# Kernel tuning notes

Measured on AMD Instinct MI355X. Metric: run time of the kernel, lower is better.

## Reference

```python
import jax, jax.numpy as jnp
import numpy as np

EMB = 768          # MineModel.emb_size
HEADS = 4          # Mi hard-codes n_heads=4 for QTLayer
DK = EMB // HEADS  # 192
H_NEED = 3         # MineModel need_num_heads
QLEN = 10000
TLEN = 3000
EG = 100000        # give edges (before head replication)
EI = 100000        # inter_1 / inter_2 edges
NLAYERS = 2


def setup_inputs() -> dict:
    key = jax.random.key(0)
    ks = jax.random.split(key, 20)
    f = lambda k, s: jax.random.normal(k, s, dtype=jnp.float32) * 0.02
    return {
        'q_emb': jax.random.normal(ks[0], (QLEN, EMB), jnp.float32),
        't_emb': jax.random.normal(ks[1], (TLEN, EMB), jnp.float32),
        'give_src': jax.random.randint(ks[2], (EG,), 0, TLEN),
        'give_dst': jax.random.randint(ks[3], (EG,), 0, QLEN),
        'i1_src': jax.random.randint(ks[4], (EI,), 0, TLEN),
        'i1_dst': jax.random.randint(ks[5], (EI,), 0, TLEN),
        'i2_src': jax.random.randint(ks[6], (EI,), 0, TLEN),
        'i2_dst': jax.random.randint(ks[7], (EI,), 0, TLEN),
        'Wq_enc': f(ks[8], (EMB, EMB * H_NEED)),
        'bq_enc': jnp.zeros((EMB * H_NEED,), jnp.float32),
        'Wc': f(ks[9], (EMB, 10)),
        'bc': jnp.zeros((10,), jnp.float32),
        'centers': f(ks[10], (10, EMB)),
        'kW': f(ks[11], (NLAYERS, 2, EMB, EMB)),
        'kb': jnp.zeros((NLAYERS, 2, EMB), jnp.float32),
        'qW': f(ks[12], (NLAYERS, 2, EMB, EMB)),
        'qb': jnp.zeros((NLAYERS, 2, EMB), jnp.float32),
        'vW': f(ks[13], (NLAYERS, 2, EMB, EMB)),
        'vb': jnp.zeros((NLAYERS, 2, EMB), jnp.float32),
        'rel_att': f(ks[14], (NLAYERS, 3, HEADS, DK, DK)),
        'rel_msg': f(ks[15], (NLAYERS, 3, HEADS, DK, DK)),
        'rel_pri': jnp.ones((NLAYERS, 3, HEADS), jnp.float32),
        'Wout': f(ks[16], (EMB, EMB)),
        'bout': jnp.zeros((EMB,), jnp.float32),
    }


def _edge_softmax(score, dst, n_dst):
    # softmax over incoming edges of each destination node, per head
    m = jax.ops.segment_max(score, dst, num_segments=n_dst)      # [N, H]
    e = jnp.exp(score - m[dst])
    s = jax.ops.segment_sum(e, dst, num_segments=n_dst)
    return e / s[dst]


def _rel(k_src, v_src, q_dst, src, dst, n_dst, ratt, rmsg, rpri):
    # HGT relation: relation-specific K/V transform, edge dot-attention, scatter-sum
    k = jnp.einsum('nhd,hde->nhe', k_src, ratt)                  # [Nsrc, H, DK]
    v = jnp.einsum('nhd,hde->nhe', v_src, rmsg)
    score = jnp.einsum('ehd,ehd->eh', q_dst[dst], k[src]) * rpri / jnp.sqrt(jnp.float32(DK))
    a = _edge_softmax(score, dst, n_dst)                         # [E, H]
    return jax.ops.segment_sum(v[src] * a[:, :, None], dst, num_segments=n_dst)


def reference(q_emb, t_emb, give_src, give_dst, i1_src, i1_dst, i2_src, i2_dst,
              Wq_enc, bq_enc, Wc, bc, centers, kW, kb, qW, qb, vW, vb,
              rel_att, rel_msg, rel_pri, Wout, bout):
    n_q = QLEN * H_NEED
    # replicate 'give' edges per model-level head (cached graph construction)
    g_src = jnp.tile(give_src, H_NEED)
    g_dst = jnp.concatenate([give_dst + QLEN * i for i in range(H_NEED)])

    # question encoder -> split heads along feature dim, concat along rows
    q_hs = q_emb @ Wq_enc + bq_enc                               # [Q, EMB*H]
    q_h = q_hs.reshape(QLEN, H_NEED, EMB).transpose(1, 0, 2).reshape(n_q, EMB)
    q_h = q_h + jnp.tile(q_emb, (H_NEED, 1))
    assign = jax.nn.softmax(q_h @ Wc + bc, axis=-1)              # [n_q, 10]
    q_h = q_h + assign @ centers

    h_tag, h_q = t_emb, q_h
    for l in range(NLAYERS):
        k_tag = (h_tag @ kW[l, 0] + kb[l, 0]).reshape(-1, HEADS, DK)
        v_tag = (h_tag @ vW[l, 0] + vb[l, 0]).reshape(-1, HEADS, DK)
        q_tag = (h_tag @ qW[l, 0] + qb[l, 0]).reshape(-1, HEADS, DK)
        q_que = (h_q @ qW[l, 1] + qb[l, 1]).reshape(-1, HEADS, DK)
        t_q = _rel(k_tag, v_tag, q_que, g_src, g_dst, n_q,
                   rel_att[l, 0], rel_msg[l, 0], rel_pri[l, 0])
        t1 = _rel(k_tag, v_tag, q_tag, i1_src, i1_dst, TLEN,
                  rel_att[l, 1], rel_msg[l, 1], rel_pri[l, 1])
        t2 = _rel(k_tag, v_tag, q_tag, i2_src, i2_dst, TLEN,
                  rel_att[l, 2], rel_msg[l, 2], rel_pri[l, 2])
        # cross_reducer='mean' over the two tag->tag relations; residual add
        h_tag = (0.5 * (t1 + t2)).reshape(-1, EMB) + h_tag
        h_q = t_q.reshape(-1, EMB) + h_q

    ques_heads = h_q @ Wout + bout                               # [H*Q, EMB]
    tags = h_tag @ Wout + bout                                   # [T, EMB]
    # torch.split(.., q_len, dim=0) + stack(dim=1) -> [Q, H, EMB]
    ques = ques_heads.reshape(H_NEED, QLEN, EMB).transpose(1, 0, 2)
    return ques, tags
```

## Files before the change

### kernel.cpp

```cpp
#include <hip/hip_runtime.h>

#define QLEN 10000
#define TLEN 3000
#define EMB 768
#define HNEED 3
#define NQ (QLEN * HNEED)
#define EG 100000
#define EI 100000
#define DKH 192
#define NHEADS 4

namespace {

typedef unsigned short u16;
typedef unsigned char u8;
typedef unsigned int u32;
typedef __attribute__((ext_vector_type(8))) short bf16x8;
typedef __attribute__((ext_vector_type(4))) float f32x4;
typedef __attribute__((ext_vector_type(2))) float f32x2;

constexpr float SCALE = 0.07216878364870322f;
constexpr long long WS = (long long)EMB * EMB;
constexpr long long RS = (long long)DKH * DKH;

__device__ inline u16 f2bf(float f) {
  unsigned u = __float_as_uint(f);
  unsigned r = (u + 0x7FFFu + ((u >> 16) & 1u)) >> 16;
  return (u16)r;
}
__device__ inline float bf2f(u16 h) {
  return __uint_as_float((unsigned)h << 16);
}
__device__ inline u8 f2fp8(float f) {
  u32 pk = __builtin_amdgcn_cvt_pk_fp8_f32(f, f, 0, false);
  return (u8)(pk & 0xFF);
}
__device__ inline void decode12(const u32* p, float* o) {
#pragma unroll
  for (int t = 0; t < 3; ++t) {
    u32 w = p[t];
    f32x2 lo = __builtin_amdgcn_cvt_pk_f32_fp8(w, false);
    f32x2 hi = __builtin_amdgcn_cvt_pk_f32_fp8(w, true);
    o[t * 4 + 0] = lo[0]; o[t * 4 + 1] = lo[1];
    o[t * 4 + 2] = hi[0]; o[t * 4 + 3] = hi[1];
  }
}
__device__ inline f32x2 bfx2(u32 w) {
  f32x2 r;
  r[0] = __uint_as_float(w << 16);
  r[1] = __uint_as_float(w & 0xFFFF0000u);
  return r;
}

__device__ inline void gload_lds16(const u16* g, u16* s) {
  __builtin_amdgcn_global_load_lds(
      (const __attribute__((address_space(1))) unsigned*)g,
      (__attribute__((address_space(3))) unsigned*)s, 16, 0, 0);
}

template <int EPI, int OUT, int MODE>
__global__ __launch_bounds__(256) void gemm_bf16(
    const u16* __restrict__ A, int lda, long long sAz,
    const u16* __restrict__ Bt, int ldb, long long sBz,
    void* __restrict__ Cv, int ldc, long long sCz,
    const float* __restrict__ bias, const u16* __restrict__ extra,
    int M, int N, int K)
{
  __shared__ __align__(16) u16 As[3][4096];
  __shared__ __align__(16) u16 Bs[3][4096];
  const int z = blockIdx.z;
  float* Cf = (float*)Cv;
  u16* Ch = (u16*)Cv;
  u8* C8 = (u8*)Cv;
  if (MODE == 1) {
    const int lr = z >> 3, kv = (z >> 2) & 1, h = z & 3;
    const int l = lr >= 3;
    A += (long long)z * RS;
    Bt = (kv ? extra : Bt) + (long long)(l * 2) * WS + h * 192;
    Ch = (u16*)Cv + (long long)lr * 1536 * 768 + (long long)(kv * 768 + h * 192) * 768;
  } else {
    A += (long long)z * sAz;
    Bt += (long long)z * sBz;
    Cf += (long long)z * sCz;
    Ch += (long long)z * sCz;
    C8 += (long long)z * sCz;
  }
  const int gx = gridDim.x;
  const int nwg = gx * gridDim.y;
  const int orig = blockIdx.y * gx + blockIdx.x;
  const int qq = nwg >> 3, rr = nwg & 7;
  const int xc = orig & 7, ix = orig >> 3;
  const int swz = (xc < rr ? xc * (qq + 1) : rr * (qq + 1) + (xc - rr) * qq) + ix;
  const int by = swz / gx, bx = swz - by * gx;
  const int bm = by * 128, bn = bx * 128;

  const int tid = threadIdx.x;
  const int w = tid >> 6, l = tid & 63;
  const int wr = w >> 1, wc = w & 1;
  const int l16 = l & 15, lk = l >> 4;
  const int srow = tid >> 2;
  const int scol = (((tid & 3) ^ ((srow >> 1) & 3))) * 8;
  const int rchunk = (lk ^ ((l16 >> 1) & 3));

  int r0 = bm + srow;      if (r0 > M - 1) r0 = M - 1;
  int r1 = bm + srow + 64; if (r1 > M - 1) r1 = M - 1;
  int c0 = bn + srow;      if (c0 > N - 1) c0 = N - 1;
  int c1 = bn + srow + 64; if (c1 > N - 1) c1 = N - 1;
  const u16* pa0 = A + (long long)r0 * lda + scol;
  const u16* pa1 = A + (long long)r1 * lda + scol;
  const u16* pb0 = Bt + (long long)c0 * ldb + scol;
  const u16* pb1 = Bt + (long long)c1 * ldb + scol;

  int aoff[4], boff[4];
#pragma unroll
  for (int m = 0; m < 4; ++m) {
    aoff[m] = (wr * 64 + m * 16 + l16) * 32 + rchunk * 8;
    boff[m] = (wc * 64 + m * 16 + l16) * 32 + rchunk * 8;
  }

  f32x4 acc[4][4] = {};
  const int nt = K / 32;

  auto stage = [&](int buf, int k0) {
    gload_lds16(pa0 + k0, &As[buf][w * 512]);
    gload_lds16(pa1 + k0, &As[buf][w * 512 + 2048]);
    gload_lds16(pb0 + k0, &Bs[buf][w * 512]);
    gload_lds16(pb1 + k0, &Bs[buf][w * 512 + 2048]);
  };

  stage(0, 0);
  stage(1, 32);
  int cur = 0, sb = 2;
  for (int t = 0; t < nt; ++t) {
    if (t < nt - 1)
      asm volatile("s_waitcnt vmcnt(4)" ::: "memory");
    else
      asm volatile("s_waitcnt vmcnt(0)" ::: "memory");
    __builtin_amdgcn_s_barrier();
    __builtin_amdgcn_sched_barrier(0);
    if (t + 2 < nt) {
      stage(sb, (t + 2) * 32);
      if (++sb == 3) sb = 0;
    }
    bf16x8 af[4], bf[4];
#pragma unroll
    for (int m = 0; m < 4; ++m)
      af[m] = *(const bf16x8*)&As[cur][aoff[m]];
#pragma unroll
    for (int n = 0; n < 4; ++n)
      bf[n] = *(const bf16x8*)&Bs[cur][boff[n]];
    __builtin_amdgcn_s_setprio(1);
#pragma unroll
    for (int m = 0; m < 4; ++m)
#pragma unroll
      for (int n = 0; n < 4; ++n)
        acc[m][n] = __builtin_amdgcn_mfma_f32_16x16x32_bf16(af[m], bf[n], acc[m][n], 0, 0, 0);
    __builtin_amdgcn_s_setprio(0);
    if (++cur == 3) cur = 0;
  }

#pragma unroll
  for (int m = 0; m < 4; ++m) {
#pragma unroll
    for (int j = 0; j < 4; ++j) {
      int grow = bm + wr * 64 + m * 16 + lk * 4 + j;
      if (grow >= M) continue;
#pragma unroll
      for (int n = 0; n < 4; ++n) {
        int gcol = bn + wc * 64 + n * 16 + l16;
        if (gcol >= N) continue;
        float val = acc[m][n][j] + (bias ? bias[gcol] : 0.f);
        if (EPI == 0) {
          if (OUT == 0)
            Cf[(long long)grow * ldc + gcol] = val;
          else if (OUT == 1)
            Ch[(long long)grow * ldc + gcol] = f2bf(val);
          else
            C8[(long long)grow * ldc + gcol] = f2fp8(val);
        } else if (EPI == 1) {
          int h = gcol / EMB, c = gcol - h * EMB;
          Ch[((long long)h * QLEN + grow) * EMB + c] =
              f2bf(val + bf2f(extra[(long long)grow * EMB + c]));
        } else {
          if (grow < NQ) {
            int i2 = grow % QLEN, h = grow / QLEN;
            Cf[((long long)i2 * HNEED + h) * EMB + gcol] = val;
          } else {
            Cf[(long long)grow * EMB + gcol] = val;
          }
        }
      }
    }
  }
}

struct PackJobs {
  const u16* A[5];
  const u16* Bt[5];
  void* C[5];
  const float* bias[5];
  int M[5];
  int nx[5];
  int ldc[5];
  int out[5];
  int start[6];
};

__global__ __launch_bounds__(256) void gemm_pack(PackJobs Jb)
{
  const int nwg = Jb.start[5];
  const int orig = blockIdx.x;
  const int qq = nwg >> 3, rr = nwg & 7;
  const int xc = orig & 7, ix = orig >> 3;
  const int swz = (xc < rr ? xc * (qq + 1) : rr * (qq + 1) + (xc - rr) * qq) + ix;
  int j = 0;
  while (swz >= Jb.start[j + 1]) ++j;
  const int local = swz - Jb.start[j];
  const int nx = Jb.nx[j];
  const int by = local / nx, bx = local - by * nx;
  const int bm = by * 128, bn = bx * 128;
  const int M = Jb.M[j];
  const int ldc = Jb.ldc[j];
  const int outk = Jb.out[j];
  const u16* A = Jb.A[j];
  const u16* Bt = Jb.Bt[j];
  const float* bias = Jb.bias[j];
  u16* Ch = (u16*)Jb.C[j];
  u8* C8 = (u8*)Jb.C[j];

  __shared__ __align__(16) u16 As[3][4096];
  __shared__ __align__(16) u16 Bs[3][4096];

  const int tid = threadIdx.x;
  const int w = tid >> 6, l = tid & 63;
  const int wr = w >> 1, wc = w & 1;
  const int l16 = l & 15, lk = l >> 4;
  const int srow = tid >> 2;
  const int scol = (((tid & 3) ^ ((srow >> 1) & 3))) * 8;
  const int rchunk = (lk ^ ((l16 >> 1) & 3));

  int r0 = bm + srow;      if (r0 > M - 1) r0 = M - 1;
  int r1 = bm + srow + 64; if (r1 > M - 1) r1 = M - 1;
  const int c0 = bn + srow;
  const int c1 = bn + srow + 64;
  const u16* pa0 = A + (long long)r0 * 768 + scol;
  const u16* pa1 = A + (long long)r1 * 768 + scol;
  const u16* pb0 = Bt + (long long)c0 * 768 + scol;
  const u16* pb1 = Bt + (long long)c1 * 768 + scol;

  int aoff[4], boff[4];
#pragma unroll
  for (int m = 0; m < 4; ++m) {
    aoff[m] = (wr * 64 + m * 16 + l16) * 32 + rchunk * 8;
    boff[m] = (wc * 64 + m * 16 + l16) * 32 + rchunk * 8;
  }

  f32x4 acc[4][4] = {};
  const int nt = 24;

  auto stage = [&](int buf, int k0) {
    gload_lds16(pa0 + k0, &As[buf][w * 512]);
    gload_lds16(pa1 + k0, &As[buf][w * 512 + 2048]);
    gload_lds16(pb0 + k0, &Bs[buf][w * 512]);
    gload_lds16(pb1 + k0, &Bs[buf][w * 512 + 2048]);
  };

  stage(0, 0);
  stage(1, 32);
  int cur = 0, sb = 2;
  for (int t = 0; t < nt; ++t) {
    if (t < nt - 1)
      asm volatile("s_waitcnt vmcnt(4)" ::: "memory");
    else
      asm volatile("s_waitcnt vmcnt(0)" ::: "memory");
    __builtin_amdgcn_s_barrier();
    __builtin_amdgcn_sched_barrier(0);
    if (t + 2 < nt) {
      stage(sb, (t + 2) * 32);
      if (++sb == 3) sb = 0;
    }
    bf16x8 af[4], bf[4];
#pragma unroll
    for (int m = 0; m < 4; ++m)
      af[m] = *(const bf16x8*)&As[cur][aoff[m]];
#pragma unroll
    for (int n = 0; n < 4; ++n)
      bf[n] = *(const bf16x8*)&Bs[cur][boff[n]];
    __builtin_amdgcn_s_setprio(1);
#pragma unroll
    for (int m = 0; m < 4; ++m)
#pragma unroll
      for (int n = 0; n < 4; ++n)
        acc[m][n] = __builtin_amdgcn_mfma_f32_16x16x32_bf16(af[m], bf[n], acc[m][n], 0, 0, 0);
    __builtin_amdgcn_s_setprio(0);
    if (++cur == 3) cur = 0;
  }

#pragma unroll
  for (int m = 0; m < 4; ++m) {
#pragma unroll
    for (int j2 = 0; j2 < 4; ++j2) {
      int grow = bm + wr * 64 + m * 16 + lk * 4 + j2;
      if (grow >= M) continue;
#pragma unroll
      for (int n = 0; n < 4; ++n) {
        int gcol = bn + wc * 64 + n * 16 + l16;
        float val = acc[m][n][j2] + bias[gcol];
        if (outk == 1)
          Ch[(long long)grow * ldc + gcol] = f2bf(val);
        else
          C8[(long long)grow * ldc + gcol] = f2fp8(val);
      }
    }
  }
}

__global__ void f2bf_kernel(const float* __restrict__ in, u16* __restrict__ out, long long n)
{
  long long i = ((long long)blockIdx.x * 256 + threadIdx.x) * 4;
  if (i >= n) return;
  float4 v = *(const float4*)(in + i);
  ushort4 o;
  o.x = f2bf(v.x); o.y = f2bf(v.y); o.z = f2bf(v.z); o.w = f2bf(v.w);
  *(ushort4*)(out + i) = o;
}

struct T12 {
  const float* s[12];
  u16* d[12];
  int ld[12];
};

__global__ __launch_bounds__(256) void transpose768(T12 jobs)
{
  const int z = blockIdx.z;
  const float* in = jobs.s[z];
  const long long ld = jobs.ld[z];
  u16* out = jobs.d[z];
  __shared__ float t[32][33];
  const int c0 = blockIdx.x * 32, r0 = blockIdx.y * 32;
  const int tx = threadIdx.x & 31, ty = threadIdx.x >> 5;
#pragma unroll
  for (int i = 0; i < 32; i += 8)
    t[ty + i][tx] = in[(long long)(r0 + ty + i) * ld + c0 + tx];
  __syncthreads();
#pragma unroll
  for (int i = 0; i < 32; i += 8)
    out[(long long)(c0 + ty + i) * 768 + r0 + tx] = f2bf(t[tx][ty + i]);
}

__global__ __launch_bounds__(256) void transpose_rel(
    const float* __restrict__ att, const float* __restrict__ msg,
    u16* __restrict__ relWT)
{
  const int z = blockIdx.z;
  const int isMsg = z >= 24;
  const int zz = isMsg ? z - 24 : z;
  const int lr = zz >> 2, h = zz & 3;
  const float* in = (isMsg ? msg : att) + (long long)zz * RS;
  u16* out = relWT + (long long)(lr * 8 + isMsg * 4 + h) * RS;
  __shared__ float t[32][33];
  const int c0 = blockIdx.x * 32, r0 = blockIdx.y * 32;
  const int tx = threadIdx.x & 31, ty = threadIdx.x >> 5;
#pragma unroll
  for (int i = 0; i < 32; i += 8)
    t[ty + i][tx] = in[(long long)(r0 + ty + i) * DKH + c0 + tx];
  __syncthreads();
#pragma unroll
  for (int i = 0; i < 32; i += 8)
    out[(long long)(c0 + ty + i) * DKH + r0 + tx] = f2bf(t[tx][ty + i]);
}

__global__ void pack_wct(const float* __restrict__ Wc, float* __restrict__ WcT)
{
  int idx = blockIdx.x * 256 + threadIdx.x;
  if (idx >= 7680) return;
  int j = idx / EMB, d = idx - j * EMB;
  WcT[idx] = Wc[d * 10 + j];
}

__global__ void bcomb_kernel(const float* __restrict__ kb, const float* __restrict__ vb,
                             const float* __restrict__ att, const float* __restrict__ msg,
                             float* __restrict__ bcomb)
{
  int idx = blockIdx.x * 256 + threadIdx.x;
  if (idx >= 6 * 1536) return;
  int lr = idx / 1536, n = idx - lr * 1536;
  int kv = n / 768, n2 = n - kv * 768;
  int h = n2 / 192, j = n2 - h * 192;
  int l = lr / 3;
  const float* bsrc = (kv ? vb : kb) + (l * 2) * EMB + h * 192;
  const float* rl = (kv ? msg : att) + ((long long)lr * 4 + h) * RS + j;
  float s = 0.f;
  for (int e = 0; e < 192; ++e) s = fmaf(bsrc[e], rl[(long long)e * 192], s);
  bcomb[idx] = s;
}

__global__ __launch_bounds__(512) void assign_center512(
    u16* __restrict__ qh_bf,
    const float* __restrict__ WcT, const float* __restrict__ bc,
    const float* __restrict__ centers)
{
  __shared__ float wc_s[7680];
  __shared__ float cen_s[7680];
  const int tid = threadIdx.x;
  for (int i = tid; i < 7680; i += 512) {
    wc_s[i] = WcT[i];
    cen_s[i] = centers[i];
  }
  __syncthreads();
  const int wave = tid >> 6, lane = tid & 63;
  const int row = blockIdx.x * 8 + wave;
  const long long base = (long long)row * EMB;
  float x[12];
#pragma unroll
  for (int i = 0; i < 12; ++i) x[i] = bf2f(qh_bf[base + lane + 64 * i]);
  float part[10] = {};
#pragma unroll
  for (int i = 0; i < 12; ++i) {
    const float v = x[i];
    const int d = lane + 64 * i;
#pragma unroll
    for (int j = 0; j < 10; ++j) part[j] = fmaf(v, wc_s[j * EMB + d], part[j]);
  }
#pragma unroll
  for (int j = 0; j < 10; ++j)
#pragma unroll
    for (int off = 32; off; off >>= 1) part[j] += __shfl_xor(part[j], off);
  float mx = -1e30f;
#pragma unroll
  for (int j = 0; j < 10; ++j) { part[j] += bc[j]; mx = fmaxf(mx, part[j]); }
  float s = 0.f;
#pragma unroll
  for (int j = 0; j < 10; ++j) { part[j] = __expf(part[j] - mx); s += part[j]; }
  const float inv = 1.f / s;
#pragma unroll
  for (int i = 0; i < 12; ++i) {
    const int d = lane + 64 * i;
    float acc = 0.f;
#pragma unroll
    for (int j = 0; j < 10; ++j) acc = fmaf(part[j], cen_s[j * EMB + d], acc);
    qh_bf[base + d] = f2bf(x[i] + acc * inv);
  }
}

__global__ void hist_all(const int* __restrict__ gd, const int* __restrict__ d1,
                         const int* __restrict__ d2, int* __restrict__ cnt)
{
  int e = blockIdx.x * 256 + threadIdx.x;
  if (e < EG) atomicAdd(&cnt[gd[e]], 1);
  else if (e < EG + EI) atomicAdd(&cnt[QLEN + d1[e - EG]], 1);
  else if (e < EG + 2 * EI) atomicAdd(&cnt[QLEN + TLEN + d2[e - EG - EI]], 1);
}

__global__ __launch_bounds__(1024) void scan3(
    const int* __restrict__ cnt_all, int* __restrict__ rp_g,
    int* __restrict__ rp_1, int* __restrict__ rp_2, int* __restrict__ cur_all)
{
  __shared__ int buf[1024];
  const int b = blockIdx.x;
  const int n = (b == 0) ? QLEN : TLEN;
  const int seg = (b == 0) ? 0 : (b == 1) ? QLEN : QLEN + TLEN;
  const int* cnt = cnt_all + seg;
  int* cur = cur_all + seg;
  int* rowptr = (b == 0) ? rp_g : (b == 1) ? rp_1 : rp_2;
  const int tid = threadIdx.x;
  const int chunk = (n + 1023) >> 10;
  const int base = tid * chunk;
  int s = 0;
  for (int i = 0; i < chunk; ++i) {
    int idx = base + i;
    if (idx < n) s += cnt[idx];
  }
  buf[tid] = s;
  __syncthreads();
  for (int off = 1; off < 1024; off <<= 1) {
    int v = (tid >= off) ? buf[tid - off] : 0;
    __syncthreads();
    buf[tid] += v;
    __syncthreads();
  }
  int run = (tid == 0) ? 0 : buf[tid - 1];
  for (int i = 0; i < chunk; ++i) {
    int idx = base + i;
    if (idx < n) {
      rowptr[idx] = run;
      cur[idx] = run;
      run += cnt[idx];
    }
  }
  if (tid == 1023) rowptr[n] = buf[1023];
}

__global__ void fill_all(const int* __restrict__ gs, const int* __restrict__ gd,
                         const int* __restrict__ s1, const int* __restrict__ d1,
                         const int* __restrict__ s2, const int* __restrict__ d2,
                         int* __restrict__ cur_all, int* __restrict__ adj_all)
{
  int e = blockIdx.x * 256 + threadIdx.x;
  if (e < EG) {
    int p = atomicAdd(&cur_all[gd[e]], 1);
    adj_all[p] = gs[e];
  } else if (e < EG + EI) {
    int p = atomicAdd(&cur_all[QLEN + d1[e - EG]], 1);
    adj_all[EG + p] = s1[e - EG];
  } else if (e < EG + 2 * EI) {
    int p = atomicAdd(&cur_all[QLEN + TLEN + d2[e - EG - EI]], 1);
    adj_all[EG + EI + p] = s2[e - EG - EI];
  }
}

__global__ __launch_bounds__(256) void gather_all(
    const u8* __restrict__ q, const u8* __restrict__ kv_g,
    const int* __restrict__ rp_g, const int* __restrict__ adj_g,
    const float* __restrict__ pri_g, u16* __restrict__ hq_bf,
    const u16* __restrict__ q_tag, const u8* __restrict__ kv1,
    const u8* __restrict__ kv2,
    const int* __restrict__ rp1, const int* __restrict__ adj1,
    const int* __restrict__ rp2, const int* __restrict__ adj2,
    const float* __restrict__ pri1, const float* __restrict__ pri2,
    u16* __restrict__ htag_bf)
{
  const int wid = blockIdx.x * 4 + (threadIdx.x >> 6);
  const int lane = threadIdx.x & 63;
  const int h = lane >> 4, sub = lane & 15;
  const int off = h * DKH + sub * 12;

  if (wid < QLEN) {
    const int d = wid;
    const int rs = rp_g[d], re = rp_g[d + 1];
    if (rs == re) return;
    const float pri = pri_g[h] * SCALE;
    float qv[3][12];
#pragma unroll
    for (int c = 0; c < 3; ++c)
      decode12((const u32*)(q + (size_t)(c * QLEN + d) * EMB + off), qv[c]);
    float S[3] = {0.f, 0.f, 0.f};
    float A[3][12] = {};
    auto edge = [&](int sn) {
      float kf[12], vf[12];
      decode12((const u32*)(kv_g + (size_t)sn * 1536 + off), kf);
      decode12((const u32*)(kv_g + (size_t)sn * 1536 + 768 + off), vf);
      float dt[3] = {0.f, 0.f, 0.f};
#pragma unroll
      for (int t = 0; t < 12; ++t) {
#pragma unroll
        for (int c = 0; c < 3; ++c) dt[c] = fmaf(qv[c][t], kf[t], dt[c]);
      }
#pragma unroll
      for (int c = 0; c < 3; ++c) {
#pragma unroll
        for (int o2 = 8; o2; o2 >>= 1) dt[c] += __shfl_xor(dt[c], o2);
        const float e = __expf(dt[c] * pri);
        S[c] += e;
#pragma unroll
        for (int t = 0; t < 12; ++t) A[c][t] = fmaf(e, vf[t], A[c][t]);
      }
    };
    int i = rs;
    for (; i + 1 < re; i += 2) { edge(adj_g[i]); edge(adj_g[i + 1]); }
    if (i < re) edge(adj_g[i]);
#pragma unroll
    for (int c = 0; c < 3; ++c) {
      const float inv = 1.f / S[c];
      u32* o = (u32*)(hq_bf + (size_t)(c * QLEN + d) * EMB + off);
#pragma unroll
      for (int t = 0; t < 6; ++t) {
        f32x2 r = bfx2(o[t]);
        r[0] += A[c][2 * t] * inv;
        r[1] += A[c][2 * t + 1] * inv;
        o[t] = (u32)f2bf(r[0]) | ((u32)f2bf(r[1]) << 16);
      }
    }
  } else {
    const int d = wid - QLEN;
    if (d >= TLEN) return;
    const int rs1 = rp1[d], re1 = rp1[d + 1];
    const int rs2 = rp2[d], re2 = rp2[d + 1];
    if (rs1 == re1 && rs2 == re2) return;
    float qv[12];
    {
      const u32* qp = (const u32*)(q_tag + (size_t)d * EMB + off);
#pragma unroll
      for (int t = 0; t < 6; ++t) {
        f32x2 r = bfx2(qp[t]);
        qv[2 * t] = r[0]; qv[2 * t + 1] = r[1];
      }
    }
    float R[12] = {};
#pragma unroll
    for (int rel = 0; rel < 2; ++rel) {
      const u8* kv = rel ? kv2 : kv1;
      const int rs = rel ? rs2 : rs1, re = rel ? re2 : re1;
      const int* adj = rel ? adj2 : adj1;
      if (rs == re) continue;
      const float pri = (rel ? pri2[h] : pri1[h]) * SCALE;
      float S = 0.f, A[12] = {};
      auto edge = [&](int sn) {
        float kf[12], vf[12];
        decode12((const u32*)(kv + (size_t)sn * 1536 + off), kf);
        decode12((const u32*)(kv + (size_t)sn * 1536 + 768 + off), vf);
        float dt = 0.f;
#pragma unroll
        for (int t = 0; t < 12; ++t) dt = fmaf(qv[t], kf[t], dt);
#pragma unroll
        for (int o2 = 8; o2; o2 >>= 1) dt += __shfl_xor(dt, o2);
        const float e = __expf(dt * pri);
        S += e;
#pragma unroll
        for (int t = 0; t < 12; ++t) A[t] = fmaf(e, vf[t], A[t]);
      };
      int i = rs;
      for (; i + 1 < re; i += 2) { edge(adj[i]); edge(adj[i + 1]); }
      if (i < re) edge(adj[i]);
      const float inv = 0.5f / S;
#pragma unroll
      for (int t = 0; t < 12; ++t) R[t] = fmaf(A[t], inv, R[t]);
    }
    u32* o = (u32*)(htag_bf + (size_t)d * EMB + off);
#pragma unroll
    for (int t = 0; t < 6; ++t) {
      f32x2 r = bfx2(o[t]);
      r[0] += R[2 * t];
      r[1] += R[2 * t + 1];
      o[t] = (u32)f2bf(r[0]) | ((u32)f2bf(r[1]) << 16);
    }
  }
}

}

extern "C" void kernel_launch(void* const* d_in, const int* in_sizes, int n_in,
                              void* d_out, int out_size, void* d_ws, size_t ws_size,
                              hipStream_t stream)
{
  const float* q_emb   = (const float*)d_in[0];
  const float* t_emb   = (const float*)d_in[1];
  const int*   give_src = (const int*)d_in[2];
  const int*   give_dst = (const int*)d_in[3];
  const int*   i1_src  = (const int*)d_in[4];
  const int*   i1_dst  = (const int*)d_in[5];
  const int*   i2_src  = (const int*)d_in[6];
  const int*   i2_dst  = (const int*)d_in[7];
  const float* Wq_enc  = (const float*)d_in[8];
  const float* bq_enc  = (const float*)d_in[9];
  const float* Wc      = (const float*)d_in[10];
  const float* bc      = (const float*)d_in[11];
  const float* centers = (const float*)d_in[12];
  const float* kW      = (const float*)d_in[13];
  const float* kb      = (const float*)d_in[14];
  const float* qW      = (const float*)d_in[15];
  const float* qb      = (const float*)d_in[16];
  const float* vW      = (const float*)d_in[17];
  const float* vb      = (const float*)d_in[18];
  const float* rel_att = (const float*)d_in[19];
  const float* rel_msg = (const float*)d_in[20];
  const float* rel_pri = (const float*)d_in[21];
  const float* Wout    = (const float*)d_in[22];
  const float* bout    = (const float*)d_in[23];
  float* out = (float*)d_out;

  float* p = (float*)d_ws;
  auto take = [&](size_t n) { float* r = p; p += ((n + 3) & ~(size_t)3); return r; };
  u16* h_q_bf    = (u16*)take((size_t)NQ * EMB / 2);
  u16* h_tag_bf  = (u16*)take((size_t)TLEN * EMB / 2);
  u16* q_emb_bf  = (u16*)take((size_t)QLEN * EMB / 2);
  u16* q_tag_bf  = (u16*)take((size_t)TLEN * EMB / 2);
  u8* kv_all     = (u8*)take((size_t)3 * TLEN * 1536 / 4);
  u8* kv_g = kv_all;
  u8* kv_1 = kv_all + (size_t)TLEN * 1536;
  u8* kv_2 = kv_all + (size_t)2 * TLEN * 1536;
  u16* WqT   = (u16*)take((size_t)3 * WS / 2);
  u16* qWT   = (u16*)take((size_t)4 * WS / 2);
  u16* WoutT = (u16*)take((size_t)WS / 2);
  u16* relWT = (u16*)take((size_t)48 * RS / 2);
  u16* kWbf  = (u16*)take((size_t)4 * WS / 2);
  u16* vWbf  = (u16*)take((size_t)4 * WS / 2);
  u16* Wcomb = (u16*)take((size_t)6 * 1536 * 768 / 2);
  float* bcomb = take(6 * 1536);
  float* WcT   = take(7680);
  int* rp_g  = (int*)take(QLEN + 1);
  int* rp_1  = (int*)take(TLEN + 1);
  int* rp_2  = (int*)take(TLEN + 1);
  int* cur_all = (int*)take(QLEN + 2 * TLEN);
  int* cnt_all = (int*)take(QLEN + 2 * TLEN);
  int* adj_all = (int*)take(EG + 2 * EI);
  int* adj_g = adj_all;
  int* adj_1 = adj_all + EG;
  int* adj_2 = adj_all + EG + EI;
  u8* q_que = (u8*)out;

  hipMemsetAsync(cnt_all, 0, (size_t)(QLEN + 2 * TLEN) * sizeof(int), stream);
  hist_all<<<(EG + 2 * EI + 255) / 256, 256, 0, stream>>>(give_dst, i1_dst, i2_dst, cnt_all);
  scan3<<<3, 1024, 0, stream>>>(cnt_all, rp_g, rp_1, rp_2, cur_all);
  fill_all<<<(EG + 2 * EI + 255) / 256, 256, 0, stream>>>(
      give_src, give_dst, i1_src, i1_dst, i2_src, i2_dst, cur_all, adj_all);

  pack_wct<<<30, 256, 0, stream>>>(Wc, WcT);
  {
    T12 jobs;
    for (int j = 0; j < 3; ++j) { jobs.s[j] = Wq_enc + j * 768; jobs.d[j] = WqT + (long long)j * WS; jobs.ld[j] = 2304; }
    for (int s = 0; s < 4; ++s) { jobs.s[3 + s] = qW + (long long)s * WS; jobs.d[3 + s] = qWT + (long long)s * WS; jobs.ld[3 + s] = 768; }
    jobs.s[7] = Wout; jobs.d[7] = WoutT; jobs.ld[7] = 768;
    for (int j = 8; j < 12; ++j) { jobs.s[j] = Wout; jobs.d[j] = WoutT; jobs.ld[j] = 768; }
    transpose768<<<dim3(24, 24, 8), 256, 0, stream>>>(jobs);
  }
  transpose_rel<<<dim3(6, 6, 48), 256, 0, stream>>>(rel_att, rel_msg, relWT);
  f2bf_kernel<<<(int)((4 * WS / 4 + 255) / 256), 256, 0, stream>>>(kW, kWbf, 4 * WS);
  f2bf_kernel<<<(int)((4 * WS / 4 + 255) / 256), 256, 0, stream>>>(vW, vWbf, 4 * WS);
  gemm_bf16<0, 1, 1><<<dim3(6, 2, 48), 256, 0, stream>>>(
      relWT, DKH, 0, kWbf, EMB, 0, Wcomb, EMB, 0, nullptr, vWbf, DKH, EMB, DKH);
  bcomb_kernel<<<36, 256, 0, stream>>>(kb, vb, rel_att, rel_msg, bcomb);

  f2bf_kernel<<<(QLEN * EMB / 4 + 255) / 256, 256, 0, stream>>>(q_emb, q_emb_bf, (long long)QLEN * EMB);
  gemm_bf16<1, 1, 0><<<dim3(18, 79, 1), 256, 0, stream>>>(
      q_emb_bf, EMB, 0, WqT, EMB, 0, h_q_bf, EMB, 0, bq_enc, q_emb_bf,
      QLEN, EMB * HNEED, EMB);
  assign_center512<<<NQ / 8, 512, 0, stream>>>(h_q_bf, WcT, bc, centers);
  f2bf_kernel<<<(TLEN * EMB / 4 + 255) / 256, 256, 0, stream>>>(t_emb, h_tag_bf, (long long)TLEN * EMB);

  for (int l = 0; l < 2; ++l) {
    PackJobs J;
    J.A[0] = h_tag_bf; J.Bt[0] = qWT + (long long)(l * 2) * WS; J.C[0] = q_tag_bf;
    J.bias[0] = qb + (l * 2) * EMB; J.M[0] = TLEN; J.nx[0] = 6; J.ldc[0] = 768; J.out[0] = 1;
    J.A[1] = h_q_bf; J.Bt[1] = qWT + (long long)(l * 2 + 1) * WS; J.C[1] = q_que;
    J.bias[1] = qb + (l * 2 + 1) * EMB; J.M[1] = NQ; J.nx[1] = 6; J.ldc[1] = 768; J.out[1] = 2;
    for (int r = 0; r < 3; ++r) {
      J.A[2 + r] = h_tag_bf;
      J.Bt[2 + r] = Wcomb + (long long)(l * 3 + r) * 1536 * 768;
      J.C[2 + r] = kv_all + (size_t)r * TLEN * 1536;
      J.bias[2 + r] = bcomb + (l * 3 + r) * 1536;
      J.M[2 + r] = TLEN; J.nx[2 + r] = 12; J.ldc[2 + r] = 1536; J.out[2 + r] = 2;
    }
    J.start[0] = 0;
    J.start[1] = 144;
    J.start[2] = 144 + 1410;
    J.start[3] = 1554 + 288;
    J.start[4] = 1842 + 288;
    J.start[5] = 2130 + 288;
    gemm_pack<<<2418, 256, 0, stream>>>(J);

    gather_all<<<(QLEN + TLEN) / 4 + 1, 256, 0, stream>>>(
        q_que, kv_g, rp_g, adj_g, rel_pri + (l * 3 + 0) * NHEADS, h_q_bf,
        q_tag_bf, kv_1, kv_2, rp_1, adj_1, rp_2, adj_2,
        rel_pri + (l * 3 + 1) * NHEADS, rel_pri + (l * 3 + 2) * NHEADS,
        h_tag_bf);
  }

  gemm_bf16<2, 0, 0><<<dim3(6, 258, 1), 256, 0, stream>>>(
      h_q_bf, EMB, 0, WoutT, EMB, 0, out, EMB, 0, bout, nullptr,
      NQ + TLEN, EMB, EMB);
}
```

Measured before the change: 761.3 us.

## Switch GEMM mainloop to BK=64 double buffering with 8-chunk XOR swizzle

Both bf16 GEMM kernels move from a three-stage, BK=32 LDS pipeline with fine-grained vmcnt waits to a two-stage, BK=64 double buffer synchronised by __syncthreads. The LDS layout uses a 64-element row with an 8-way XOR chunk swizzle, and each stage issues four loads per operand per thread. The aim is to halve the number of barriers per K and do more MFMA work per sync. In exchange, prefetch depth drops to one stage, and the full __syncthreads may wait on outstanding loads, which can expose memory latency. The N-bound clamp on B rows is also dropped in the generic kernel.

```diff
diff --git a/kernel.cpp b/kernel.cpp
--- a/kernel.cpp
+++ b/kernel.cpp
@@ -66,17 +66,17 @@
     const float* __restrict__ bias, const u16* __restrict__ extra,
     int M, int N, int K)
 {
-  __shared__ __align__(16) u16 As[3][4096];
-  __shared__ __align__(16) u16 Bs[3][4096];
+  __shared__ __align__(16) u16 As[2][8192];
+  __shared__ __align__(16) u16 Bs[2][8192];
   const int z = blockIdx.z;
   float* Cf = (float*)Cv;
   u16* Ch = (u16*)Cv;
   u8* C8 = (u8*)Cv;
   if (MODE == 1) {
     const int lr = z >> 3, kv = (z >> 2) & 1, h = z & 3;
-    const int l = lr >= 3;
+    const int l2 = lr >= 3;
     A += (long long)z * RS;
-    Bt = (kv ? extra : Bt) + (long long)(l * 2) * WS + h * 192;
+    Bt = (kv ? extra : Bt) + (long long)(l2 * 2) * WS + h * 192;
     Ch = (u16*)Cv + (long long)lr * 1536 * 768 + (long long)(kv * 768 + h * 192) * 768;
   } else {
     A += (long long)z * sAz;
@@ -98,65 +98,64 @@
   const int w = tid >> 6, l = tid & 63;
   const int wr = w >> 1, wc = w & 1;
   const int l16 = l & 15, lk = l >> 4;
-  const int srow = tid >> 2;
-  const int scol = (((tid & 3) ^ ((srow >> 1) & 3))) * 8;
-  const int rchunk = (lk ^ ((l16 >> 1) & 3));
-
-  int r0 = bm + srow;      if (r0 > M - 1) r0 = M - 1;
-  int r1 = bm + srow + 64; if (r1 > M - 1) r1 = M - 1;
-  int c0 = bn + srow;      if (c0 > N - 1) c0 = N - 1;
-  int c1 = bn + srow + 64; if (c1 > N - 1) c1 = N - 1;
-  const u16* pa0 = A + (long long)r0 * lda + scol;
-  const u16* pa1 = A + (long long)r1 * lda + scol;
-  const u16* pb0 = Bt + (long long)c0 * ldb + scol;
-  const u16* pb1 = Bt + (long long)c1 * ldb + scol;
-
-  int aoff[4], boff[4];
-#pragma unroll
-  for (int m = 0; m < 4; ++m) {
-    aoff[m] = (wr * 64 + m * 16 + l16) * 32 + rchunk * 8;
-    boff[m] = (wc * 64 + m * 16 + l16) * 32 + rchunk * 8;
-  }
+  const int lrow = l >> 3;
+  const int lchunk = l & 7;
+  const int gcol = ((lchunk ^ lrow) * 8);
+
+  const u16* pa[4];
+  const u16* pb[4];
+#pragma unroll
+  for (int pp = 0; pp < 4; ++pp) {
+    int ra = bm + w * 8 + lrow + pp * 32; if (ra > M - 1) ra = M - 1;
+    int rb = bn + w * 8 + lrow + pp * 32;
+    pa[pp] = A + (long long)ra * lda + gcol;
+    pb[pp] = Bt + (long long)rb * ldb + gcol;
+  }
+
+  int aoff[2][4], boff[2][4];
+#pragma unroll
+  for (int ks = 0; ks < 2; ++ks)
+#pragma unroll
+    for (int m = 0; m < 4; ++m) {
+      aoff[ks][m] = (wr * 64 + m * 16 + l16) * 64 + (((lk + ks * 4) ^ (l16 & 7)) * 8);
+      boff[ks][m] = (wc * 64 + m * 16 + l16) * 64 + (((lk + ks * 4) ^ (l16 & 7)) * 8);
+    }
 
   f32x4 acc[4][4] = {};
-  const int nt = K / 32;
+  const int nt = K / 64;
 
   auto stage = [&](int buf, int k0) {
-    gload_lds16(pa0 + k0, &As[buf][w * 512]);
-    gload_lds16(pa1 + k0, &As[buf][w * 512 + 2048]);
-    gload_lds16(pb0 + k0, &Bs[buf][w * 512]);
-    gload_lds16(pb1 + k0, &Bs[buf][w * 512 + 2048]);
+#pragma unroll
+    for (int pp = 0; pp < 4; ++pp) {
+      gload_lds16(pa[pp] + k0, &As[buf][(w * 8 + pp * 32) * 64]);
+      gload_lds16(pb[pp] + k0, &Bs[buf][(w * 8 + pp * 32) * 64]);
+    }
   };
 
   stage(0, 0);
-  stage(1, 32);
-  int cur = 0, sb = 2;
+  __syncthreads();
+  int cur = 0;
   for (int t = 0; t < nt; ++t) {
-    if (t < nt - 1)
-      asm volatile("s_waitcnt vmcnt(4)" ::: "memory");
-    else
-      asm volatile("s_waitcnt vmcnt(0)" ::: "memory");
-    __builtin_amdgcn_s_barrier();
-    __builtin_amdgcn_sched_barrier(0);
-    if (t + 2 < nt) {
-      stage(sb, (t + 2) * 32);
-      if (++sb == 3) sb = 0;
-    }
-    bf16x8 af[4], bf[4];
-#pragma unroll
-    for (int m = 0; m < 4; ++m)
-      af[m] = *(const bf16x8*)&As[cur][aoff[m]];
-#pragma unroll
-    for (int n = 0; n < 4; ++n)
-      bf[n] = *(const bf16x8*)&Bs[cur][boff[n]];
-    __builtin_amdgcn_s_setprio(1);
-#pragma unroll
-    for (int m = 0; m < 4; ++m)
+    if (t + 1 < nt) stage(cur ^ 1, (t + 1) * 64);
+#pragma unroll
+    for (int ks = 0; ks < 2; ++ks) {
+      bf16x8 af[4], bf[4];
+#pragma unroll
+      for (int m = 0; m < 4; ++m)
+        af[m] = *(const bf16x8*)&As[cur][aoff[ks][m]];
 #pragma unroll
       for (int n = 0; n < 4; ++n)
-        acc[m][n] = __builtin_amdgcn_mfma_f32_16x16x32_bf16(af[m], bf[n], acc[m][n], 0, 0, 0);
-    __builtin_amdgcn_s_setprio(0);
-    if (++cur == 3) cur = 0;
+        bf[n] = *(const bf16x8*)&Bs[cur][boff[ks][n]];
+      __builtin_amdgcn_s_setprio(1);
+#pragma unroll
+      for (int m = 0; m < 4; ++m)
+#pragma unroll
+        for (int n = 0; n < 4; ++n)
+          acc[m][n] = __builtin_amdgcn_mfma_f32_16x16x32_bf16(af[m], bf[n], acc[m][n], 0, 0, 0);
+      __builtin_amdgcn_s_setprio(0);
+    }
+    __syncthreads();
+    cur ^= 1;
   }
 
 #pragma unroll
@@ -167,26 +166,26 @@
       if (grow >= M) continue;
 #pragma unroll
       for (int n = 0; n < 4; ++n) {
-        int gcol = bn + wc * 64 + n * 16 + l16;
-        if (gcol >= N) continue;
-        float val = acc[m][n][j] + (bias ? bias[gcol] : 0.f);
+        int gcol2 = bn + wc * 64 + n * 16 + l16;
+        if (gcol2 >= N) continue;
+        float val = acc[m][n][j] + (bias ? bias[gcol2] : 0.f);
         if (EPI == 0) {
           if (OUT == 0)
-            Cf[(long long)grow * ldc + gcol] = val;
+            Cf[(long long)grow * ldc + gcol2] = val;
           else if (OUT == 1)
-            Ch[(long long)grow * ldc + gcol] = f2bf(val);
+            Ch[(long long)grow * ldc + gcol2] = f2bf(val);
           else
-            C8[(long long)grow * ldc + gcol] = f2fp8(val);
+            C8[(long long)grow * ldc + gcol2] = f2fp8(val);
         } else if (EPI == 1) {
-          int h = gcol / EMB, c = gcol - h * EMB;
+          int h = gcol2 / EMB, c = gcol2 - h * EMB;
           Ch[((long long)h * QLEN + grow) * EMB + c] =
               f2bf(val + bf2f(extra[(long long)grow * EMB + c]));
         } else {
           if (grow < NQ) {
             int i2 = grow % QLEN, h = grow / QLEN;
-            Cf[((long long)i2 * HNEED + h) * EMB + gcol] = val;
+            Cf[((long long)i2 * HNEED + h) * EMB + gcol2] = val;
           } else {
-            Cf[(long long)grow * EMB + gcol] = val;
+            Cf[(long long)grow * EMB + gcol2] = val;
           }
         }
       }
@@ -228,72 +227,71 @@
   u16* Ch = (u16*)Jb.C[j];
   u8* C8 = (u8*)Jb.C[j];
 
-  __shared__ __align__(16) u16 As[3][4096];
-  __shared__ __align__(16) u16 Bs[3][4096];
+  __shared__ __align__(16) u16 As[2][8192];
+  __shared__ __align__(16) u16 Bs[2][8192];
 
   const int tid = threadIdx.x;
   const int w = tid >> 6, l = tid & 63;
   const int wr = w >> 1, wc = w & 1;
   const int l16 = l & 15, lk = l >> 4;
-  const int srow = tid >> 2;
-  const int scol = (((tid & 3) ^ ((srow >> 1) & 3))) * 8;
-  const int rchunk = (lk ^ ((l16 >> 1) & 3));
-
-  int r0 = bm + srow;      if (r0 > M - 1) r0 = M - 1;
-  int r1 = bm + srow + 64; if (r1 > M - 1) r1 = M - 1;
-  const int c0 = bn + srow;
-  const int c1 = bn + srow + 64;
-  const u16* pa0 = A + (long long)r0 * 768 + scol;
-  const u16* pa1 = A + (long long)r1 * 768 + scol;
-  const u16* pb0 = Bt + (long long)c0 * 768 + scol;
-  const u16* pb1 = Bt + (long long)c1 * 768 + scol;
-
-  int aoff[4], boff[4];
-#pragma unroll
-  for (int m = 0; m < 4; ++m) {
-    aoff[m] = (wr * 64 + m * 16 + l16) * 32 + rchunk * 8;
-    boff[m] = (wc * 64 + m * 16 + l16) * 32 + rchunk * 8;
-  }
+  const int lrow = l >> 3;
+  const int lchunk = l & 7;
+  const int gcol = ((lchunk ^ lrow) * 8);
+
+  const u16* pa[4];
+  const u16* pb[4];
+#pragma unroll
+  for (int pp = 0; pp < 4; ++pp) {
+    int ra = bm + w * 8 + lrow + pp * 32; if (ra > M - 1) ra = M - 1;
+    int rb = bn + w * 8 + lrow + pp * 32;
+    pa[pp] = A + (long long)ra * 768 + gcol;
+    pb[pp] = Bt + (long long)rb * 768 + gcol;
+  }
+
+  int aoff[2][4], boff[2][4];
+#pragma unroll
+  for (int ks = 0; ks < 2; ++ks)
+#pragma unroll
+    for (int m = 0; m < 4; ++m) {
+      aoff[ks][m] = (wr * 64 + m * 16 + l16) * 64 + (((lk + ks * 4) ^ (l16 & 7)) * 8);
+      boff[ks][m] = (wc * 64 + m * 16 + l16) * 64 + (((lk + ks * 4) ^ (l16 & 7)) * 8);
+    }
 
   f32x4 acc[4][4] = {};
-  const int nt = 24;
+  const int nt = 12;
 
   auto stage = [&](int buf, int k0) {
-    gload_lds16(pa0 + k0, &As[buf][w * 512]);
-    gload_lds16(pa1 + k0, &As[buf][w * 512 + 2048]);
-    gload_lds16(pb0 + k0, &Bs[buf][w * 512]);
-    gload_lds16(pb1 + k0, &Bs[buf][w * 512 + 2048]);
+#pragma unroll
+    for (int pp = 0; pp < 4; ++pp) {
+      gload_lds16(pa[pp] + k0, &As[buf][(w * 8 + pp * 32) * 64]);
+      gload_lds16(pb[pp] + k0, &Bs[buf][(w * 8 + pp * 32) * 64]);
+    }
   };
 
   stage(0, 0);
-  stage(1, 32);
-  int cur = 0, sb = 2;
+  __syncthreads();
+  int cur = 0;
   for (int t = 0; t < nt; ++t) {
-    if (t < nt - 1)
-      asm volatile("s_waitcnt vmcnt(4)" ::: "memory");
-    else
-      asm volatile("s_waitcnt vmcnt(0)" ::: "memory");
-    __builtin_amdgcn_s_barrier();
-    __builtin_amdgcn_sched_barrier(0);
-    if (t + 2 < nt) {
-      stage(sb, (t + 2) * 32);
-      if (++sb == 3) sb = 0;
-    }
-    bf16x8 af[4], bf[4];
-#pragma unroll
-    for (int m = 0; m < 4; ++m)
-      af[m] = *(const bf16x8*)&As[cur][aoff[m]];
-#pragma unroll
-    for (int n = 0; n < 4; ++n)
-      bf[n] = *(const bf16x8*)&Bs[cur][boff[n]];
-    __builtin_amdgcn_s_setprio(1);
-#pragma unroll
-    for (int m = 0; m < 4; ++m)
+    if (t + 1 < nt) stage(cur ^ 1, (t + 1) * 64);
+#pragma unroll
+    for (int ks = 0; ks < 2; ++ks) {
+      bf16x8 af[4], bf[4];
+#pragma unroll
+      for (int m = 0; m < 4; ++m)
+        af[m] = *(const bf16x8*)&As[cur][aoff[ks][m]];
 #pragma unroll
       for (int n = 0; n < 4; ++n)
-        acc[m][n] = __builtin_amdgcn_mfma_f32_16x16x32_bf16(af[m], bf[n], acc[m][n], 0, 0, 0);
-    __builtin_amdgcn_s_setprio(0);
-    if (++cur == 3) cur = 0;
+        bf[n] = *(const bf16x8*)&Bs[cur][boff[ks][n]];
+      __builtin_amdgcn_s_setprio(1);
+#pragma unroll
+      for (int m = 0; m < 4; ++m)
+#pragma unroll
+        for (int n = 0; n < 4; ++n)
+          acc[m][n] = __builtin_amdgcn_mfma_f32_16x16x32_bf16(af[m], bf[n], acc[m][n], 0, 0, 0);
+      __builtin_amdgcn_s_setprio(0);
+    }
+    __syncthreads();
+    cur ^= 1;
   }
 
 #pragma unroll
@@ -304,12 +302,12 @@
       if (grow >= M) continue;
 #pragma unroll
       for (int n = 0; n < 4; ++n) {
-        int gcol = bn + wc * 64 + n * 16 + l16;
-        float val = acc[m][n][j2] + bias[gcol];
+        int gcol2 = bn + wc * 64 + n * 16 + l16;
+        float val = acc[m][n][j2] + bias[gcol2];
         if (outk == 1)
-          Ch[(long long)grow * ldc + gcol] = f2bf(val);
+          Ch[(long long)grow * ldc + gcol2] = f2bf(val);
         else
-          C8[(long long)grow * ldc + gcol] = f2fp8(val);
+          C8[(long long)grow * ldc + gcol2] = f2fp8(val);
       }
     }
   }
```

Result: slower. 793.5 us (+4.2%).

## Load B operand directly into registers instead of staging through LDS

Applied to the files above, without the earlier changes.

Both GEMM kernels stop staging the B tile through shared memory. Each lane now loads its own MFMA B fragments straight from global memory into registers, prefetching one k-step ahead. A is still staged through LDS, now double-buffered instead of triple-buffered. This cuts LDS footprint and LDS read traffic, but the uncoalesced per-lane B loads from global/L2 are duplicated across the two warp rows, and A prefetch depth drops from two stages to one.

```diff
diff --git a/kernel.cpp b/kernel.cpp
--- a/kernel.cpp
+++ b/kernel.cpp
@@ -66,17 +66,16 @@
     const float* __restrict__ bias, const u16* __restrict__ extra,
     int M, int N, int K)
 {
-  __shared__ __align__(16) u16 As[3][4096];
-  __shared__ __align__(16) u16 Bs[3][4096];
+  __shared__ __align__(16) u16 As[2][4096];
   const int z = blockIdx.z;
   float* Cf = (float*)Cv;
   u16* Ch = (u16*)Cv;
   u8* C8 = (u8*)Cv;
   if (MODE == 1) {
     const int lr = z >> 3, kv = (z >> 2) & 1, h = z & 3;
-    const int l = lr >= 3;
+    const int l2 = lr >= 3;
     A += (long long)z * RS;
-    Bt = (kv ? extra : Bt) + (long long)(l * 2) * WS + h * 192;
+    Bt = (kv ? extra : Bt) + (long long)(l2 * 2) * WS + h * 192;
     Ch = (u16*)Cv + (long long)lr * 1536 * 768 + (long long)(kv * 768 + h * 192) * 768;
   } else {
     A += (long long)z * sAz;
@@ -104,59 +103,66 @@
 
   int r0 = bm + srow;      if (r0 > M - 1) r0 = M - 1;
   int r1 = bm + srow + 64; if (r1 > M - 1) r1 = M - 1;
-  int c0 = bn + srow;      if (c0 > N - 1) c0 = N - 1;
-  int c1 = bn + srow + 64; if (c1 > N - 1) c1 = N - 1;
   const u16* pa0 = A + (long long)r0 * lda + scol;
   const u16* pa1 = A + (long long)r1 * lda + scol;
-  const u16* pb0 = Bt + (long long)c0 * ldb + scol;
-  const u16* pb1 = Bt + (long long)c1 * ldb + scol;
-
-  int aoff[4], boff[4];
-#pragma unroll
-  for (int m = 0; m < 4; ++m) {
+
+  const u16* pB[4];
+#pragma unroll
+  for (int n = 0; n < 4; ++n) {
+    int cb = bn + wc * 64 + n * 16 + l16;
+    if (cb > N - 1) cb = N - 1;
+    pB[n] = Bt + (long long)cb * ldb + lk * 8;
+  }
+
+  int aoff[4];
+#pragma unroll
+  for (int m = 0; m < 4; ++m)
     aoff[m] = (wr * 64 + m * 16 + l16) * 32 + rchunk * 8;
-    boff[m] = (wc * 64 + m * 16 + l16) * 32 + rchunk * 8;
-  }
 
   f32x4 acc[4][4] = {};
   const int nt = K / 32;
 
-  auto stage = [&](int buf, int k0) {
+  auto stageA = [&](int buf, int k0) {
     gload_lds16(pa0 + k0, &As[buf][w * 512]);
     gload_lds16(pa1 + k0, &As[buf][w * 512 + 2048]);
-    gload_lds16(pb0 + k0, &Bs[buf][w * 512]);
-    gload_lds16(pb1 + k0, &Bs[buf][w * 512 + 2048]);
   };
 
-  stage(0, 0);
-  stage(1, 32);
-  int cur = 0, sb = 2;
+  bf16x8 bcur[4], bnxt[4];
+  stageA(0, 0);
+#pragma unroll
+  for (int n = 0; n < 4; ++n) bcur[n] = *(const bf16x8*)(pB[n]);
+  asm volatile("s_waitcnt vmcnt(0)" ::: "memory");
+  __builtin_amdgcn_s_barrier();
+  __builtin_amdgcn_sched_barrier(0);
+
+  int cur = 0;
   for (int t = 0; t < nt; ++t) {
-    if (t < nt - 1)
+    if (t + 1 < nt) {
+#pragma unroll
+      for (int n = 0; n < 4; ++n) bnxt[n] = *(const bf16x8*)(pB[n] + (t + 1) * 32);
       asm volatile("s_waitcnt vmcnt(4)" ::: "memory");
-    else
+    } else {
       asm volatile("s_waitcnt vmcnt(0)" ::: "memory");
+    }
     __builtin_amdgcn_s_barrier();
     __builtin_amdgcn_sched_barrier(0);
-    if (t + 2 < nt) {
-      stage(sb, (t + 2) * 32);
-      if (++sb == 3) sb = 0;
-    }
-    bf16x8 af[4], bf[4];
+    if (t + 1 < nt) stageA(cur ^ 1, (t + 1) * 32);
+    bf16x8 af[4];
 #pragma unroll
     for (int m = 0; m < 4; ++m)
       af[m] = *(const bf16x8*)&As[cur][aoff[m]];
-#pragma unroll
-    for (int n = 0; n < 4; ++n)
-      bf[n] = *(const bf16x8*)&Bs[cur][boff[n]];
     __builtin_amdgcn_s_setprio(1);
 #pragma unroll
     for (int m = 0; m < 4; ++m)
 #pragma unroll
       for (int n = 0; n < 4; ++n)
-        acc[m][n] = __builtin_amdgcn_mfma_f32_16x16x32_bf16(af[m], bf[n], acc[m][n], 0, 0, 0);
+        acc[m][n] = __builtin_amdgcn_mfma_f32_16x16x32_bf16(af[m], bcur[n], acc[m][n], 0, 0, 0);
     __builtin_amdgcn_s_setprio(0);
-    if (++cur == 3) cur = 0;
+    if (t + 1 < nt) {
+#pragma unroll
+      for (int n = 0; n < 4; ++n) bcur[n] = bnxt[n];
+    }
+    cur ^= 1;
   }
 
 #pragma unroll
@@ -167,26 +173,26 @@
       if (grow >= M) continue;
 #pragma unroll
       for (int n = 0; n < 4; ++n) {
-        int gcol = bn + wc * 64 + n * 16 + l16;
-        if (gcol >= N) continue;
-        float val = acc[m][n][j] + (bias ? bias[gcol] : 0.f);
+        int gcol2 = bn + wc * 64 + n * 16 + l16;
+        if (gcol2 >= N) continue;
+        float val = acc[m][n][j] + (bias ? bias[gcol2] : 0.f);
         if (EPI == 0) {
           if (OUT == 0)
-            Cf[(long long)grow * ldc + gcol] = val;
+            Cf[(long long)grow * ldc + gcol2] = val;
           else if (OUT == 1)
-            Ch[(long long)grow * ldc + gcol] = f2bf(val);
+            Ch[(long long)grow * ldc + gcol2] = f2bf(val);
           else
-            C8[(long long)grow * ldc + gcol] = f2fp8(val);
+            C8[(long long)grow * ldc + gcol2] = f2fp8(val);
         } else if (EPI == 1) {
-          int h = gcol / EMB, c = gcol - h * EMB;
+          int h = gcol2 / EMB, c = gcol2 - h * EMB;
           Ch[((long long)h * QLEN + grow) * EMB + c] =
               f2bf(val + bf2f(extra[(long long)grow * EMB + c]));
         } else {
           if (grow < NQ) {
             int i2 = grow % QLEN, h = grow / QLEN;
-            Cf[((long long)i2 * HNEED + h) * EMB + gcol] = val;
+            Cf[((long long)i2 * HNEED + h) * EMB + gcol2] = val;
           } else {
-            Cf[(long long)grow * EMB + gcol] = val;
+            Cf[(long long)grow * EMB + gcol2] = val;
           }
         }
       }
@@ -228,8 +234,7 @@
   u16* Ch = (u16*)Jb.C[j];
   u8* C8 = (u8*)Jb.C[j];
 
-  __shared__ __align__(16) u16 As[3][4096];
-  __shared__ __align__(16) u16 Bs[3][4096];
+  __shared__ __align__(16) u16 As[2][4096];
 
   const int tid = threadIdx.x;
   const int w = tid >> 6, l = tid & 63;
@@ -241,59 +246,65 @@
 
   int r0 = bm + srow;      if (r0 > M - 1) r0 = M - 1;
   int r1 = bm + srow + 64; if (r1 > M - 1) r1 = M - 1;
-  const int c0 = bn + srow;
-  const int c1 = bn + srow + 64;
   const u16* pa0 = A + (long long)r0 * 768 + scol;
   const u16* pa1 = A + (long long)r1 * 768 + scol;
-  const u16* pb0 = Bt + (long long)c0 * 768 + scol;
-  const u16* pb1 = Bt + (long long)c1 * 768 + scol;
-
-  int aoff[4], boff[4];
-#pragma unroll
-  for (int m = 0; m < 4; ++m) {
+
+  const u16* pB[4];
+#pragma unroll
+  for (int n = 0; n < 4; ++n) {
+    int cb = bn + wc * 64 + n * 16 + l16;
+    pB[n] = Bt + (long long)cb * 768 + lk * 8;
+  }
+
+  int aoff[4];
+#pragma unroll
+  for (int m = 0; m < 4; ++m)
     aoff[m] = (wr * 64 + m * 16 + l16) * 32 + rchunk * 8;
-    boff[m] = (wc * 64 + m * 16 + l16) * 32 + rchunk * 8;
-  }
 
   f32x4 acc[4][4] = {};
   const int nt = 24;
 
-  auto stage = [&](int buf, int k0) {
+  auto stageA = [&](int buf, int k0) {
     gload_lds16(pa0 + k0, &As[buf][w * 512]);
     gload_lds16(pa1 + k0, &As[buf][w * 512 + 2048]);
-    gload_lds16(pb0 + k0, &Bs[buf][w * 512]);
-    gload_lds16(pb1 + k0, &Bs[buf][w * 512 + 2048]);
   };
 
-  stage(0, 0);
-  stage(1, 32);
-  int cur = 0, sb = 2;
+  bf16x8 bcur[4], bnxt[4];
+  stageA(0, 0);
+#pragma unroll
+  for (int n = 0; n < 4; ++n) bcur[n] = *(const bf16x8*)(pB[n]);
+  asm volatile("s_waitcnt vmcnt(0)" ::: "memory");
+  __builtin_amdgcn_s_barrier();
+  __builtin_amdgcn_sched_barrier(0);
+
+  int cur = 0;
   for (int t = 0; t < nt; ++t) {
-    if (t < nt - 1)
+    if (t + 1 < nt) {
+#pragma unroll
+      for (int n = 0; n < 4; ++n) bnxt[n] = *(const bf16x8*)(pB[n] + (t + 1) * 32);
       asm volatile("s_waitcnt vmcnt(4)" ::: "memory");
-    else
+    } else {
       asm volatile("s_waitcnt vmcnt(0)" ::: "memory");
+    }
     __builtin_amdgcn_s_barrier();
     __builtin_amdgcn_sched_barrier(0);
-    if (t + 2 < nt) {
-      stage(sb, (t + 2) * 32);
-      if (++sb == 3) sb = 0;
-    }
-    bf16x8 af[4], bf[4];
+    if (t + 1 < nt) stageA(cur ^ 1, (t + 1) * 32);
+    bf16x8 af[4];
 #pragma unroll
     for (int m = 0; m < 4; ++m)
       af[m] = *(const bf16x8*)&As[cur][aoff[m]];
-#pragma unroll
-    for (int n = 0; n < 4; ++n)
-      bf[n] = *(const bf16x8*)&Bs[cur][boff[n]];
     __builtin_amdgcn_s_setprio(1);
 #pragma unroll
     for (int m = 0; m < 4; ++m)
 #pragma unroll
       for (int n = 0; n < 4; ++n)
-        acc[m][n] = __builtin_amdgcn_mfma_f32_16x16x32_bf16(af[m], bf[n], acc[m][n], 0, 0, 0);
+        acc[m][n] = __builtin_amdgcn_mfma_f32_16x16x32_bf16(af[m], bcur[n], acc[m][n], 0, 0, 0);
     __builtin_amdgcn_s_setprio(0);
-    if (++cur == 3) cur = 0;
+    if (t + 1 < nt) {
+#pragma unroll
+      for (int n = 0; n < 4; ++n) bcur[n] = bnxt[n];
+    }
+    cur ^= 1;
   }
 
 #pragma unroll
@@ -304,12 +315,12 @@
       if (grow >= M) continue;
 #pragma unroll
       for (int n = 0; n < 4; ++n) {
-        int gcol = bn + wc * 64 + n * 16 + l16;
-        float val = acc[m][n][j2] + bias[gcol];
+        int gcol2 = bn + wc * 64 + n * 16 + l16;
+        float val = acc[m][n][j2] + bias[gcol2];
         if (outk == 1)
-          Ch[(long long)grow * ldc + gcol] = f2bf(val);
+          Ch[(long long)grow * ldc + gcol2] = f2bf(val);
         else
-          C8[(long long)grow * ldc + gcol] = f2fp8(val);
+          C8[(long long)grow * ldc + gcol2] = f2fp8(val);
       }
     }
   }
```

After: 927.8 us. 21.9% more time.
